# Kernel optimization log

Hardware: AMD Instinct MI355X
Metric: run time of the kernel (lower is better)

## Reference

```python
import jax, jax.numpy as jnp
import numpy as np

N_HEAD = 12
EPS = 1e-6


def setup_inputs() -> dict:
    key = jax.random.key(0)
    k1, k2, k3 = jax.random.split(key, 3)
    B, T, C = 2, 2048, 768
    x = jax.random.normal(k1, (B, T, C), dtype=jnp.float32)
    c_attn_w = jax.random.normal(k2, (3 * C, C), dtype=jnp.float32) * 0.02
    c_proj_w = jax.random.normal(k3, (C, C), dtype=jnp.float32) * 0.02
    temperature = jnp.ones((1,), dtype=jnp.float32) * np.sqrt(C // N_HEAD)
    return {"x": x, "c_attn_w": c_attn_w, "c_proj_w": c_proj_w, "temperature": temperature}


def reference(x, c_attn_w, c_proj_w, temperature):
    B, T, C = x.shape
    H = N_HEAD
    D = C // H
    qkv = x @ c_attn_w.T  # [B,T,3C] (no bias)
    q, k, v = jnp.split(qkv, 3, axis=2)
    # [B,H,T,D]
    q = q.reshape(B, T, H, D).transpose(0, 2, 1, 3)
    k = k.reshape(B, T, H, D).transpose(0, 2, 1, 3)
    v = v.reshape(B, T, H, D).transpose(0, 2, 1, 3)

    # autocorrelation via FFT along time axis, zero-padded to 2T
    fft_len = 2 * T
    q_fft = jnp.fft.rfft(q, n=fft_len, axis=2)
    k_fft = jnp.fft.rfft(k, n=fft_len, axis=2)
    corr = jnp.fft.irfft(q_fft * jnp.conj(k_fft), n=fft_len, axis=2)[:, :, :T, :]
    corr_weights = corr.mean(axis=-1) / (temperature + EPS)  # [B,H,T] over lag

    # causal lag mask: position t may use lags 0..t
    t_idx = jnp.arange(T)
    lag_mask = t_idx[None, :] <= t_idx[:, None]  # [T(pos), T(lag)]
    weights_masked = jnp.where(lag_mask[None, None], corr_weights[:, :, None, :], -jnp.inf)
    attn = jax.nn.softmax(weights_masked, axis=-1)  # [B,H,T,T] over lags
    attn = jnp.nan_to_num(attn)

    # Original gathers v at source position s = clamp(t - lag, 0), producing a
    # (B,H,T,T,D) tensor. Since lags > t have zero weight, this is exactly
    # y[t] = sum_{s<=t} attn[t, t-s] * v[s]. Build the position-score matrix by
    # gathering attn along the lag axis — avoids the 5D blowup, same math.
    lag_idx = jnp.clip(t_idx[:, None] - t_idx[None, :], 0)  # [T(pos), T(src)]
    scores = jnp.take_along_axis(attn, lag_idx[None, None], axis=-1)
    scores = jnp.where(lag_mask[None, None], scores, 0.0)  # zero out s > t
    y = jnp.einsum('bhts,bhsd->bhtd', scores, v)

    y = y.transpose(0, 2, 1, 3).reshape(B, T, C)
    return y @ c_proj_w.T
```

## Files before the change

kernel.cpp:

```cpp
#include <hip/hip_runtime.h>

#define T_ 2048
#define B_ 2
#define H_ 12
#define C_ 768
#define M_ 4096
#define BH_ (B_ * H_)
#define RSTR 2200

typedef __attribute__((ext_vector_type(4))) float f32x4;
typedef __attribute__((ext_vector_type(16))) float f32x16;
typedef __attribute__((ext_vector_type(8))) __bf16 bf16x8;
typedef __attribute__((ext_vector_type(4))) __bf16 bf16x4;

#define GLOAD16(GP, LP)                                                   \
  __builtin_amdgcn_global_load_lds(                                       \
      (__attribute__((address_space(1))) void*)(GP),                      \
      (__attribute__((address_space(3))) void*)(LP), 16, 0, 0)


__global__ __launch_bounds__(256) void cvt3_k(const float* __restrict__ x,
                                              const float* __restrict__ ca,
                                              const float* __restrict__ cp,
                                              __bf16* __restrict__ xb,
                                              __bf16* __restrict__ wb,
                                              __bf16* __restrict__ pb) {
  const int id = blockIdx.x;
  const float* src;
  __bf16* dst;
  size_t base;
  if (id < 1536) { src = x; dst = xb; base = (size_t)id * 2048; }
  else if (id < 2400) { src = ca; dst = wb; base = (size_t)(id - 1536) * 2048; }
  else { src = cp; dst = pb; base = (size_t)(id - 2400) * 2048; }
  const size_t o = base + (size_t)threadIdx.x * 8;
  f32x4 v0 = *(const f32x4*)(src + o);
  f32x4 v1 = *(const f32x4*)(src + o + 4);
  bf16x8 r;
#pragma unroll
  for (int j = 0; j < 4; ++j) { r[j] = (__bf16)v0[j]; r[4 + j] = (__bf16)v1[j]; }
  *(bf16x8*)(dst + o) = r;
}

__global__ __launch_bounds__(256) void gemm_qkv(const __bf16* __restrict__ A,
                                                const __bf16* __restrict__ Bm,
                                                __bf16* __restrict__ Qp,
                                                __bf16* __restrict__ Kp,
                                                __bf16* __restrict__ Vp) {
  __shared__ __align__(16) __bf16 sA[4096];
  __shared__ __align__(16) __bf16 sB[4096];
  const int tid = threadIdx.x;
  const int id = blockIdx.x;
  const int lg = (id & 7) * 72 + (id >> 3);
  const int m0 = (lg / 18) * 128, n0 = (lg % 18) * 128;
  const int lane = tid & 63, w = tid >> 6;
  const int wr = w >> 1, wc = w & 1;
  const int fr = lane & 15;
  const int ko = (lane >> 4) << 3;
  const int srow = lane >> 2, scol = (lane & 3) << 3;
  const __bf16* Ab = A + (size_t)(m0 + srow) * 768 + scol;
  const __bf16* Bb = Bm + (size_t)(n0 + srow) * 768 + scol;
  const int c0 = 2 * w, c1 = 2 * w + 1;
  f32x4 acc[4][4] = {};
  for (int k0 = 0; k0 < 768; k0 += 32) {
    GLOAD16(Ab + (size_t)c0 * 16 * 768 + k0, &sA[c0 * 512]);
    GLOAD16(Ab + (size_t)c1 * 16 * 768 + k0, &sA[c1 * 512]);
    GLOAD16(Bb + (size_t)c0 * 16 * 768 + k0, &sB[c0 * 512]);
    GLOAD16(Bb + (size_t)c1 * 16 * 768 + k0, &sB[c1 * 512]);
    __syncthreads();
    bf16x8 a[4], b[4];
#pragma unroll
    for (int m = 0; m < 4; ++m) a[m] = *(const bf16x8*)&sA[(wr * 64 + m * 16 + fr) * 32 + ko];
#pragma unroll
    for (int n = 0; n < 4; ++n) b[n] = *(const bf16x8*)&sB[(wc * 64 + n * 16 + fr) * 32 + ko];
#pragma unroll
    for (int m = 0; m < 4; ++m)
#pragma unroll
      for (int n = 0; n < 4; ++n)
        acc[m][n] = __builtin_amdgcn_mfma_f32_16x16x32_bf16(a[m], b[n], acc[m][n], 0, 0, 0);
    __syncthreads();
  }
  const int orow = (lane >> 4) << 2, ocol = lane & 15;
#pragma unroll
  for (int m = 0; m < 4; ++m)
#pragma unroll
    for (int n = 0; n < 4; ++n) {
      int r = m0 + wr * 64 + m * 16 + orow;
      int c = n0 + wc * 64 + n * 16 + ocol;
      int sec = c / 768;
      int hd = c - sec * 768;
      int h = hd >> 6, d = hd & 63;
      int b = r >> 11, t = r & 2047;
      int bh = b * H_ + h;
      if (sec < 2) {
        int tile = t >> 5, rr = t & 31;
        int kc = d >> 4, half = (d >> 3) & 1, dj = d & 7;
        __bf16* dst = (sec == 0 ? Qp : Kp) + ((size_t)bh * 64 + tile) * 2048 +
                      kc * 512 + (half * 32 + rr) * 8 + dj;
#pragma unroll
        for (int j = 0; j < 4; ++j) dst[j * 8] = (__bf16)acc[m][n][j];
      } else {
        int chunk = t >> 6, sk = t & 63;
        int kc = sk >> 4, hf = (sk >> 3) & 1, j0 = sk & 7;
        bf16x4 pk;
#pragma unroll
        for (int j = 0; j < 4; ++j) pk[j] = (__bf16)acc[m][n][j];
        *(bf16x4*)(Vp + ((size_t)bh * 32 + chunk) * 4096 + (d >> 5) * 2048 +
                   kc * 512 + (hf * 32 + (d & 31)) * 8 + j0) = pk;
      }
    }
}

__global__ __launch_bounds__(256) void gemm_out(const __bf16* __restrict__ A,
                                                const __bf16* __restrict__ Bm,
                                                float* __restrict__ C) {
  __shared__ __align__(16) __bf16 sA[4096];
  __shared__ __align__(16) __bf16 sB[4096];
  const int tid = threadIdx.x;
  const int id = blockIdx.x;
  const int lg = (id & 7) * 24 + (id >> 3);
  const int m0 = (lg / 6) * 128, n0 = (lg % 6) * 128;
  const int lane = tid & 63, w = tid >> 6;
  const int wr = w >> 1, wc = w & 1;
  const int fr = lane & 15;
  const int ko = (lane >> 4) << 3;
  const int srow = lane >> 2, scol = (lane & 3) << 3;
  const __bf16* Ab = A + (size_t)(m0 + srow) * 768 + scol;
  const __bf16* Bb = Bm + (size_t)(n0 + srow) * 768 + scol;
  const int c0 = 2 * w, c1 = 2 * w + 1;
  f32x4 acc[4][4] = {};
  for (int k0 = 0; k0 < 768; k0 += 32) {
    GLOAD16(Ab + (size_t)c0 * 16 * 768 + k0, &sA[c0 * 512]);
    GLOAD16(Ab + (size_t)c1 * 16 * 768 + k0, &sA[c1 * 512]);
    GLOAD16(Bb + (size_t)c0 * 16 * 768 + k0, &sB[c0 * 512]);
    GLOAD16(Bb + (size_t)c1 * 16 * 768 + k0, &sB[c1 * 512]);
    __syncthreads();
    bf16x8 a[4], b[4];
#pragma unroll
    for (int m = 0; m < 4; ++m) a[m] = *(const bf16x8*)&sA[(wr * 64 + m * 16 + fr) * 32 + ko];
#pragma unroll
    for (int n = 0; n < 4; ++n) b[n] = *(const bf16x8*)&sB[(wc * 64 + n * 16 + fr) * 32 + ko];
#pragma unroll
    for (int m = 0; m < 4; ++m)
#pragma unroll
      for (int n = 0; n < 4; ++n)
        acc[m][n] = __builtin_amdgcn_mfma_f32_16x16x32_bf16(a[m], b[n], acc[m][n], 0, 0, 0);
    __syncthreads();
  }
  const int orow = (lane >> 4) << 2, ocol = lane & 15;
#pragma unroll
  for (int m = 0; m < 4; ++m)
#pragma unroll
    for (int n = 0; n < 4; ++n) {
      int r = m0 + wr * 64 + m * 16 + orow;
      int c = n0 + wc * 64 + n * 16 + ocol;
#pragma unroll
      for (int j = 0; j < 4; ++j) C[(size_t)(r + j) * 768 + c] = acc[m][n][j];
    }
}

__global__ __launch_bounds__(256) void corr_mfma(const __bf16* __restrict__ Qp,
                                                 const __bf16* __restrict__ Kp,
                                                 __bf16* __restrict__ Cw) {
  const int tid = threadIdx.x;
  int id = blockIdx.x;
  int sub = id >> 3;
  const int bh = (id & 7) * 3 + sub / 36;
  const int pi = sub % 36;
  int x = pi, qb = 0;
  while (x >= 8 - qb) { x -= 8 - qb; ++qb; }
  const int tc = qb + x;
  const int lane = tid & 63, w = tid >> 6;

  const __bf16* qp = Qp + ((size_t)bh << 17) + (lane << 3);
  const __bf16* kp = Kp + ((size_t)bh << 17) + (lane << 3);
  const int qA = 8 * qb + 2 * w;
  f32x16 acc0 = {}, acc1 = {};
  const bf16x8 zf = {};
  bf16x8 Af[2][4], Kc[2][4], Kpv[4];

  {
    const int t0 = 8 * tc;
#pragma unroll
    for (int kc = 0; kc < 4; ++kc) Af[0][kc] = *(const bf16x8*)(qp + t0 * 2048 + kc * 512);
    const int s0 = t0 - qA, sm = s0 - 1;
#pragma unroll
    for (int kc = 0; kc < 4; ++kc) {
      Kc[0][kc] = (s0 >= 0) ? *(const bf16x8*)(kp + s0 * 2048 + kc * 512) : zf;
      Kpv[kc] = (sm >= 0) ? *(const bf16x8*)(kp + sm * 2048 + kc * 512) : zf;
    }
  }
#pragma unroll
  for (int ii = 0; ii < 8; ++ii) {
    const int cur = ii & 1, nxt = cur ^ 1;
    if (ii < 7) {
      const int tn = 8 * tc + ii + 1;
      const int sn = tn - qA;
#pragma unroll
      for (int kc = 0; kc < 4; ++kc) {
        Af[nxt][kc] = *(const bf16x8*)(qp + tn * 2048 + kc * 512);
        Kc[nxt][kc] = (sn >= 0) ? *(const bf16x8*)(kp + sn * 2048 + kc * 512) : zf;
      }
    }
#pragma unroll
    for (int kc = 0; kc < 4; ++kc) {
      acc0 = __builtin_amdgcn_mfma_f32_32x32x16_bf16(Af[cur][kc], Kc[cur][kc], acc0, 0, 0, 0);
      acc1 = __builtin_amdgcn_mfma_f32_32x32x16_bf16(Af[cur][kc], Kpv[kc], acc1, 0, 0, 0);
    }
#pragma unroll
    for (int kc = 0; kc < 4; ++kc) Kpv[kc] = Kc[cur][kc];
  }

  __bf16* o = Cw + (((size_t)(bh * 36 + pi) * 4 + w) * 2) * 1024 + lane;
#pragma unroll
  for (int j = 0; j < 16; ++j) {
    o[j * 64] = (__bf16)acc0[j];
    o[1024 + j * 64] = (__bf16)acc1[j];
  }
}

__global__ __launch_bounds__(256) void corr_red(const __bf16* __restrict__ Cw,
                                                float* __restrict__ P12) {
  __shared__ float tile[4][1056];
  __shared__ float prow[4][2112];
  const int id = blockIdx.x;
  const int bh = id % 24, g = id / 24;
  const int tid = threadIdx.x, lane = tid & 63, w = tid >> 6;

  for (int i = tid; i < 4 * 2112; i += 256) ((float*)prow)[i] = 0.f;
  __syncthreads();

  const int col = lane & 31, hi = lane >> 5;
#pragma unroll
  for (int pp = 0; pp < 3; ++pp) {
    const int pi = g * 3 + pp;
    int x = pi, qb = 0;
    while (x >= 8 - qb) { x -= 8 - qb; ++qb; }
#pragma unroll
    for (int b01 = 0; b01 < 2; ++b01) {
      const __bf16* src =
          Cw + (((size_t)(bh * 36 + pi) * 4 + w) * 2 + b01) * 1024 + lane;
      float v[16];
#pragma unroll
      for (int j = 0; j < 16; ++j) v[j] = (float)src[j * 64];
#pragma unroll
      for (int j = 0; j < 16; ++j) {
        int row = (j & 3) + ((j >> 2) << 3) + 4 * hi;
        tile[w][row * 33 + col] = v[j];
      }
      __syncthreads();
      if (lane < 63) {
        const int d = lane - 31;
        float s = 0.f;
#pragma unroll
        for (int c = 0; c < 32; ++c) {
          int r = c + d;
          bool ok = (unsigned)r < 32u;
          float val = tile[w][(ok ? r : 0) * 33 + c];
          s += ok ? val : 0.f;
        }
        const int qA = 8 * qb + 2 * w + b01;
        prow[w][32 * qA + d + 32] += s;
      }
      __syncthreads();
    }
  }

  float* out = P12 + ((size_t)g * BH_ + bh) * T_;
  float ov[8];
#pragma unroll
  for (int u = 0; u < 8; ++u) {
    int L = (tid << 3) + u;
    ov[u] = prow[0][L + 32] + prow[1][L + 32] + prow[2][L + 32] + prow[3][L + 32];
  }
  *(f32x4*)(out + (tid << 3)) = *(f32x4*)&ov[0];
  *(f32x4*)(out + (tid << 3) + 4) = *(f32x4*)&ov[4];
}

__global__ __launch_bounds__(256) void soft_k(const float* __restrict__ P,
                                              const float* __restrict__ temp,
                                              __bf16* __restrict__ Rb,
                                              float* __restrict__ zinv) {
  __shared__ float se[T_];
  __shared__ float lm[4], wsum[4];
  const int bh = blockIdx.x, tid = threadIdx.x;
  const int lane = tid & 63, wid = tid >> 6;
  const float scale = 1.0f / (64.0f * (temp[0] + 1e-6f));
  f32x4 sa = {}, sb = {};
#pragma unroll
  for (int j = 0; j < 12; ++j) {
    const float* pp = P + ((size_t)j * BH_ + bh) * T_ + (tid << 3);
    sa += *(const f32x4*)pp;
    sb += *(const f32x4*)(pp + 4);
  }
  float v[8];
#pragma unroll
  for (int i = 0; i < 4; ++i) { v[i] = sa[i] * scale; v[4 + i] = sb[i] * scale; }
  float m = v[0];
#pragma unroll
  for (int i = 1; i < 8; ++i) m = fmaxf(m, v[i]);
#pragma unroll
  for (int off = 1; off < 64; off <<= 1) m = fmaxf(m, __shfl_xor(m, off));
  if (lane == 0) lm[wid] = m;
  __syncthreads();
  m = fmaxf(fmaxf(lm[0], lm[1]), fmaxf(lm[2], lm[3]));
  float ex[8], pr[8], run = 0;
#pragma unroll
  for (int i = 0; i < 8; ++i) { ex[i] = __expf(v[i] - m); run += ex[i]; pr[i] = run; }
  float s = run;
  for (int off = 1; off < 64; off <<= 1) {
    float o = __shfl_up(s, off);
    if (lane >= off) s += o;
  }
  if (lane == 63) wsum[wid] = s;
  __syncthreads();
  float base = s - run;
  for (int jw = 0; jw < wid; ++jw) base += wsum[jw];
#pragma unroll
  for (int i = 0; i < 8; ++i) {
    int t = (tid << 3) + i;
    zinv[(size_t)bh * T_ + t] = 1.0f / (base + pr[i]);
    se[t] = ex[i];
  }
  __syncthreads();
  __bf16* rb = Rb + (size_t)bh * 8 * RSTR;
  for (int c = tid; c < RSTR / 8; c += 256) {
    int i0 = c << 3;
#pragma unroll
    for (int p = 0; p < 8; ++p) {
      bf16x8 ovv;
#pragma unroll
      for (int e = 0; e < 8; ++e) {
        int idx = T_ - 1 - p - (i0 + e);
        ovv[e] = (__bf16)((idx >= 0) ? se[idx] : 0.f);
      }
      *(bf16x8*)(rb + p * RSTR + i0) = ovv;
    }
  }
}

__global__ __launch_bounds__(256) void conv_k(const __bf16* __restrict__ Vp,
                                              const __bf16* __restrict__ Rb,
                                              const float* __restrict__ zinv,
                                              __bf16* __restrict__ y2b) {
  __shared__ __align__(16) __bf16 revc[8 * RSTR];
  const int tid = threadIdx.x;
  int id = blockIdx.x;
  int sub = id >> 3;
  const int bh = (id & 7) * 3 + (sub >> 4);
  const int pr = sub & 15;
  const int lane = tid & 63, w = tid >> 6;

  const __bf16* rb = Rb + (size_t)bh * 8 * RSTR;
  for (int c = tid; c < RSTR; c += 256)
    *(bf16x8*)&revc[c << 3] = *(const bf16x8*)(rb + ((size_t)c << 3));
  __syncthreads();

  const int fr = lane & 31, kg = (lane >> 5) << 3;
  const int tt = (w < 2) ? (64 * pr + 32 * w) : (64 * (31 - pr) + 32 * (w - 2));
  const int trow = tt + fr;
  const int pp = (T_ - 1 - trow) & 7;
  const int obase = (T_ - 1 - trow) - pp;
  const __bf16* vpb = Vp + (size_t)bh * 131072 + (lane << 3);
  f32x16 acc0 = {}, acc1 = {};
  const int nst = (tt >> 6) + 1;

  bf16x8 A00, A01, A02, A03, A10, A11, A12, A13;
  bf16x8 B00, B01, B02, B03, B10, B11, B12, B13;
  bf16x8 C00, C01, C02, C03, C10, C11, C12, C13;

#define LOADV(P, CH)                                                          \
  {                                                                           \
    const __bf16* vb_ = vpb + (size_t)(CH) * 4096;                            \
    P##00 = *(const bf16x8*)(vb_);          P##01 = *(const bf16x8*)(vb_ + 512);  \
    P##02 = *(const bf16x8*)(vb_ + 1024);   P##03 = *(const bf16x8*)(vb_ + 1536); \
    P##10 = *(const bf16x8*)(vb_ + 2048);   P##11 = *(const bf16x8*)(vb_ + 2560); \
    P##12 = *(const bf16x8*)(vb_ + 3072);   P##13 = *(const bf16x8*)(vb_ + 3584); \
  }
#define MSTEP(P, ST)                                                          \
  {                                                                           \
    const int ab_ = pp * RSTR + obase + (ST) * 64 + kg;                       \
    bf16x8 a0_ = *(const bf16x8*)&revc[ab_];                                  \
    bf16x8 a1_ = *(const bf16x8*)&revc[ab_ + 16];                             \
    bf16x8 a2_ = *(const bf16x8*)&revc[ab_ + 32];                             \
    bf16x8 a3_ = *(const bf16x8*)&revc[ab_ + 48];                             \
    acc0 = __builtin_amdgcn_mfma_f32_32x32x16_bf16(a0_, P##00, acc0, 0, 0, 0);\
    acc1 = __builtin_amdgcn_mfma_f32_32x32x16_bf16(a0_, P##10, acc1, 0, 0, 0);\
    acc0 = __builtin_amdgcn_mfma_f32_32x32x16_bf16(a1_, P##01, acc0, 0, 0, 0);\
    acc1 = __builtin_amdgcn_mfma_f32_32x32x16_bf16(a1_, P##11, acc1, 0, 0, 0);\
    acc0 = __builtin_amdgcn_mfma_f32_32x32x16_bf16(a2_, P##02, acc0, 0, 0, 0);\
    acc1 = __builtin_amdgcn_mfma_f32_32x32x16_bf16(a2_, P##12, acc1, 0, 0, 0);\
    acc0 = __builtin_amdgcn_mfma_f32_32x32x16_bf16(a3_, P##03, acc0, 0, 0, 0);\
    acc1 = __builtin_amdgcn_mfma_f32_32x32x16_bf16(a3_, P##13, acc1, 0, 0, 0);\
  }

  LOADV(A, 0);
  if (nst > 1) LOADV(B, 1);
  if (nst > 2) LOADV(C, 2);
  int st = 0;
  while (true) {
    MSTEP(A, st); if (st + 3 < nst) LOADV(A, st + 3); if (++st >= nst) break;
    MSTEP(B, st); if (st + 3 < nst) LOADV(B, st + 3); if (++st >= nst) break;
    MSTEP(C, st); if (st + 3 < nst) LOADV(C, st + 3); if (++st >= nst) break;
  }
#undef LOADV
#undef MSTEP

  const int b = bh / H_, h = bh % H_;
  const int ocol = lane & 31, rbj = (lane >> 5) << 2;
  const float* zp = zinv + (size_t)bh * T_;
#pragma unroll
  for (int j = 0; j < 16; ++j) {
    int row = (j & 3) + ((j >> 2) << 3) + rbj;
    int t = tt + row;
    float zi = zp[t];
    __bf16* yr = y2b + ((size_t)b * T_ + t) * C_ + h * 64;
    yr[ocol] = (__bf16)(acc0[j] * zi);
    yr[32 + ocol] = (__bf16)(acc1[j] * zi);
  }
}

extern "C" void kernel_launch(void* const* d_in, const int* in_sizes, int n_in,
                              void* d_out, int out_size, void* d_ws, size_t ws_size,
                              hipStream_t stream) {
  const float* x = (const float*)d_in[0];
  const float* c_attn = (const float*)d_in[1];
  const float* c_proj = (const float*)d_in[2];
  const float* temp = (const float*)d_in[3];
  float* out = (float*)d_out;

  __bf16* Qp = (__bf16*)d_ws;
  __bf16* Kp = Qp + (size_t)3145728;
  __bf16* Vp = Kp + (size_t)3145728;
  __bf16* Rb = Vp + (size_t)3145728;
  float* zinv = (float*)(Rb + 422400);
  float* P12 = zinv + 49152;
  __bf16* pb = (__bf16*)(P12 + 589824);
  __bf16* zone = pb + 589824;
  __bf16* xb = zone;
  __bf16* wb = zone + 3145728;
  __bf16* Cw = zone;
  __bf16* y2b = zone;

  cvt3_k<<<dim3(2688), 256, 0, stream>>>(x, c_attn, c_proj, xb, wb, pb);
  gemm_qkv<<<dim3(576), 256, 0, stream>>>(xb, wb, Qp, Kp, Vp);
  corr_mfma<<<dim3(864), 256, 0, stream>>>(Qp, Kp, Cw);
  corr_red<<<dim3(288), 256, 0, stream>>>(Cw, P12);
  soft_k<<<dim3(BH_), 256, 0, stream>>>(P12, temp, Rb, zinv);
  conv_k<<<dim3(384), 256, 0, stream>>>(Vp, Rb, zinv, y2b);
  gemm_out<<<dim3(192), 256, 0, stream>>>(y2b, pb, out);
}
```

Before: 110.9 us.

## Fuse correlation reduction into MFMA kernel and shrink output GEMM tiles

The diagonal-sum reduction now runs inside the correlation MFMA kernel, straight from the accumulators through LDS. This removes the bf16 intermediate round trip to global memory and one kernel launch. Each block writes a full-length partial row per pair index (36 partials instead of 12), so soft_k now sums 36 slices, adding more global traffic there. The output GEMM also moves from 128x128 to 64x64 tiles, raising the block count from 192 to 768 to fill more CUs at the cost of less reuse per block.

Measured after the change: 94.85 us. -14.5%, faster.

```diff
diff --git a/kernel.cpp b/kernel.cpp
--- a/kernel.cpp
+++ b/kernel.cpp
@@ -113,54 +113,53 @@
 __global__ __launch_bounds__(256) void gemm_out(const __bf16* __restrict__ A,
                                                 const __bf16* __restrict__ Bm,
                                                 float* __restrict__ C) {
-  __shared__ __align__(16) __bf16 sA[4096];
-  __shared__ __align__(16) __bf16 sB[4096];
+  __shared__ __align__(16) __bf16 sA[2048];
+  __shared__ __align__(16) __bf16 sB[2048];
   const int tid = threadIdx.x;
   const int id = blockIdx.x;
-  const int lg = (id & 7) * 24 + (id >> 3);
-  const int m0 = (lg / 6) * 128, n0 = (lg % 6) * 128;
+  const int lg = (id & 7) * 96 + (id >> 3);
+  const int m0 = (lg / 12) * 64, n0 = (lg % 12) * 64;
   const int lane = tid & 63, w = tid >> 6;
   const int wr = w >> 1, wc = w & 1;
   const int fr = lane & 15;
   const int ko = (lane >> 4) << 3;
-  const int srow = lane >> 2, scol = (lane & 3) << 3;
+  const int srow = tid >> 2, scol = (tid & 3) << 3;
   const __bf16* Ab = A + (size_t)(m0 + srow) * 768 + scol;
   const __bf16* Bb = Bm + (size_t)(n0 + srow) * 768 + scol;
-  const int c0 = 2 * w, c1 = 2 * w + 1;
-  f32x4 acc[4][4] = {};
+  f32x4 acc[2][2] = {};
   for (int k0 = 0; k0 < 768; k0 += 32) {
-    GLOAD16(Ab + (size_t)c0 * 16 * 768 + k0, &sA[c0 * 512]);
-    GLOAD16(Ab + (size_t)c1 * 16 * 768 + k0, &sA[c1 * 512]);
-    GLOAD16(Bb + (size_t)c0 * 16 * 768 + k0, &sB[c0 * 512]);
-    GLOAD16(Bb + (size_t)c1 * 16 * 768 + k0, &sB[c1 * 512]);
-    __syncthreads();
-    bf16x8 a[4], b[4];
-#pragma unroll
-    for (int m = 0; m < 4; ++m) a[m] = *(const bf16x8*)&sA[(wr * 64 + m * 16 + fr) * 32 + ko];
-#pragma unroll
-    for (int n = 0; n < 4; ++n) b[n] = *(const bf16x8*)&sB[(wc * 64 + n * 16 + fr) * 32 + ko];
-#pragma unroll
-    for (int m = 0; m < 4; ++m)
-#pragma unroll
-      for (int n = 0; n < 4; ++n)
+    GLOAD16(Ab + k0, &sA[w * 512]);
+    GLOAD16(Bb + k0, &sB[w * 512]);
+    __syncthreads();
+    bf16x8 a[2], b[2];
+#pragma unroll
+    for (int m = 0; m < 2; ++m) a[m] = *(const bf16x8*)&sA[(wr * 32 + m * 16 + fr) * 32 + ko];
+#pragma unroll
+    for (int n = 0; n < 2; ++n) b[n] = *(const bf16x8*)&sB[(wc * 32 + n * 16 + fr) * 32 + ko];
+#pragma unroll
+    for (int m = 0; m < 2; ++m)
+#pragma unroll
+      for (int n = 0; n < 2; ++n)
         acc[m][n] = __builtin_amdgcn_mfma_f32_16x16x32_bf16(a[m], b[n], acc[m][n], 0, 0, 0);
     __syncthreads();
   }
   const int orow = (lane >> 4) << 2, ocol = lane & 15;
 #pragma unroll
-  for (int m = 0; m < 4; ++m)
-#pragma unroll
-    for (int n = 0; n < 4; ++n) {
-      int r = m0 + wr * 64 + m * 16 + orow;
-      int c = n0 + wc * 64 + n * 16 + ocol;
+  for (int m = 0; m < 2; ++m)
+#pragma unroll
+    for (int n = 0; n < 2; ++n) {
+      int r = m0 + wr * 32 + m * 16 + orow;
+      int c = n0 + wc * 32 + n * 16 + ocol;
 #pragma unroll
       for (int j = 0; j < 4; ++j) C[(size_t)(r + j) * 768 + c] = acc[m][n][j];
     }
 }
 
-__global__ __launch_bounds__(256) void corr_mfma(const __bf16* __restrict__ Qp,
-                                                 const __bf16* __restrict__ Kp,
-                                                 __bf16* __restrict__ Cw) {
+__global__ __launch_bounds__(256) void corr_k2(const __bf16* __restrict__ Qp,
+                                               const __bf16* __restrict__ Kp,
+                                               float* __restrict__ P36) {
+  __shared__ float tile[4][1056];
+  __shared__ float prow[4][288];
   const int tid = threadIdx.x;
   int id = blockIdx.x;
   int sub = id >> 3;
@@ -171,6 +170,8 @@
   const int tc = qb + x;
   const int lane = tid & 63, w = tid >> 6;
 
+  for (int i = tid; i < 4 * 288; i += 256) ((float*)prow)[i] = 0.f;
+
   const __bf16* qp = Qp + ((size_t)bh << 17) + (lane << 3);
   const __bf16* kp = Kp + ((size_t)bh << 17) + (lane << 3);
   const int qA = 8 * qb + 2 * w;
@@ -210,70 +211,45 @@
     for (int kc = 0; kc < 4; ++kc) Kpv[kc] = Kc[cur][kc];
   }
 
-  __bf16* o = Cw + (((size_t)(bh * 36 + pi) * 4 + w) * 2) * 1024 + lane;
-#pragma unroll
-  for (int j = 0; j < 16; ++j) {
-    o[j * 64] = (__bf16)acc0[j];
-    o[1024 + j * 64] = (__bf16)acc1[j];
-  }
-}
-
-__global__ __launch_bounds__(256) void corr_red(const __bf16* __restrict__ Cw,
-                                                float* __restrict__ P12) {
-  __shared__ float tile[4][1056];
-  __shared__ float prow[4][2112];
-  const int id = blockIdx.x;
-  const int bh = id % 24, g = id / 24;
-  const int tid = threadIdx.x, lane = tid & 63, w = tid >> 6;
-
-  for (int i = tid; i < 4 * 2112; i += 256) ((float*)prow)[i] = 0.f;
+  const int col = lane & 31, hi = lane >> 5;
+  const int d = lane - 31;
   __syncthreads();
-
-  const int col = lane & 31, hi = lane >> 5;
-#pragma unroll
-  for (int pp = 0; pp < 3; ++pp) {
-    const int pi = g * 3 + pp;
-    int x = pi, qb = 0;
-    while (x >= 8 - qb) { x -= 8 - qb; ++qb; }
-#pragma unroll
-    for (int b01 = 0; b01 < 2; ++b01) {
-      const __bf16* src =
-          Cw + (((size_t)(bh * 36 + pi) * 4 + w) * 2 + b01) * 1024 + lane;
-      float v[16];
-#pragma unroll
-      for (int j = 0; j < 16; ++j) v[j] = (float)src[j * 64];
-#pragma unroll
-      for (int j = 0; j < 16; ++j) {
-        int row = (j & 3) + ((j >> 2) << 3) + 4 * hi;
-        tile[w][row * 33 + col] = v[j];
+#pragma unroll
+  for (int b01 = 0; b01 < 2; ++b01) {
+    const f32x16* ac = (b01 == 0) ? &acc0 : &acc1;
+#pragma unroll
+    for (int j = 0; j < 16; ++j) {
+      int row = (j & 3) + ((j >> 2) << 3) + 4 * hi;
+      tile[w][row * 33 + col] = (*ac)[j];
+    }
+    __syncthreads();
+    if (lane < 63) {
+      float s = 0.f;
+#pragma unroll
+      for (int c = 0; c < 32; ++c) {
+        int r = c + d;
+        bool ok = (unsigned)r < 32u;
+        float val = tile[w][(ok ? r : 0) * 33 + c];
+        s += ok ? val : 0.f;
       }
-      __syncthreads();
-      if (lane < 63) {
-        const int d = lane - 31;
-        float s = 0.f;
-#pragma unroll
-        for (int c = 0; c < 32; ++c) {
-          int r = c + d;
-          bool ok = (unsigned)r < 32u;
-          float val = tile[w][(ok ? r : 0) * 33 + c];
-          s += ok ? val : 0.f;
-        }
-        const int qA = 8 * qb + 2 * w + b01;
-        prow[w][32 * qA + d + 32] += s;
-      }
-      __syncthreads();
-    }
-  }
-
-  float* out = P12 + ((size_t)g * BH_ + bh) * T_;
+      prow[w][32 * (2 * w + b01) + d + 32] += s;
+    }
+    __syncthreads();
+  }
+
+  float* Pd = P36 + ((size_t)pi * BH_ + bh) * T_;
   float ov[8];
 #pragma unroll
   for (int u = 0; u < 8; ++u) {
     int L = (tid << 3) + u;
-    ov[u] = prow[0][L + 32] + prow[1][L + 32] + prow[2][L + 32] + prow[3][L + 32];
-  }
-  *(f32x4*)(out + (tid << 3)) = *(f32x4*)&ov[0];
-  *(f32x4*)(out + (tid << 3) + 4) = *(f32x4*)&ov[4];
+    int l = L - 256 * qb;
+    float s = 0.f;
+    if (l >= -31 && l < 256)
+      s = prow[0][l + 32] + prow[1][l + 32] + prow[2][l + 32] + prow[3][l + 32];
+    ov[u] = s;
+  }
+  *(f32x4*)(Pd + (tid << 3)) = *(f32x4*)&ov[0];
+  *(f32x4*)(Pd + (tid << 3) + 4) = *(f32x4*)&ov[4];
 }
 
 __global__ __launch_bounds__(256) void soft_k(const float* __restrict__ P,
@@ -287,7 +263,7 @@
   const float scale = 1.0f / (64.0f * (temp[0] + 1e-6f));
   f32x4 sa = {}, sb = {};
 #pragma unroll
-  for (int j = 0; j < 12; ++j) {
+  for (int j = 0; j < 36; ++j) {
     const float* pp = P + ((size_t)j * BH_ + bh) * T_ + (tid << 3);
     sa += *(const f32x4*)pp;
     sb += *(const f32x4*)(pp + 4);
@@ -433,19 +409,16 @@
   __bf16* Vp = Kp + (size_t)3145728;
   __bf16* Rb = Vp + (size_t)3145728;
   float* zinv = (float*)(Rb + 422400);
-  float* P12 = zinv + 49152;
-  __bf16* pb = (__bf16*)(P12 + 589824);
-  __bf16* zone = pb + 589824;
-  __bf16* xb = zone;
-  __bf16* wb = zone + 3145728;
-  __bf16* Cw = zone;
-  __bf16* y2b = zone;
+  float* P36 = zinv + 49152;
+  __bf16* pb = (__bf16*)(P36 + 1769472);
+  __bf16* xb = pb + 589824;
+  __bf16* wb = xb + 3145728;
+  __bf16* y2b = xb;
 
   cvt3_k<<<dim3(2688), 256, 0, stream>>>(x, c_attn, c_proj, xb, wb, pb);
   gemm_qkv<<<dim3(576), 256, 0, stream>>>(xb, wb, Qp, Kp, Vp);
-  corr_mfma<<<dim3(864), 256, 0, stream>>>(Qp, Kp, Cw);
-  corr_red<<<dim3(288), 256, 0, stream>>>(Cw, P12);
-  soft_k<<<dim3(BH_), 256, 0, stream>>>(P12, temp, Rb, zinv);
+  corr_k2<<<dim3(864), 256, 0, stream>>>(Qp, Kp, P36);
+  soft_k<<<dim3(BH_), 256, 0, stream>>>(P36, temp, Rb, zinv);
   conv_k<<<dim3(384), 256, 0, stream>>>(Vp, Rb, zinv, y2b);
-  gemm_out<<<dim3(192), 256, 0, stream>>>(y2b, pb, out);
-}
+  gemm_out<<<dim3(768), 256, 0, stream>>>(y2b, pb, out);
+}
```
